# Kernel tuning notes

Measured on AMD Instinct MI355X. Metric: run time of the kernel, lower is better.

The kernel has to match this reference:

```python
import jax, jax.numpy as jnp
import numpy as np


def _skew_relative(QE):
    # QE: [B, H, N, 2N-1] -> [B, H, N, N] relative-position skew (Music-Transformer style)
    B, H, N, L = QE.shape  # L == 2N - 1
    x = jnp.pad(QE, ((0, 0), (0, 0), (0, 0), (0, 1))).reshape(B, H, N * (L + 1))
    x = jnp.pad(x, ((0, 0), (0, 0), (0, N - 1))).reshape(B, H, N + 1, 2 * N - 1)
    return x[:, :, :N, -N:]


def setup_inputs() -> dict:
    key = jax.random.key(0)
    ks = jax.random.split(key, 8)
    B, N, D, H, dh = 8, 1024, 512, 8, 64
    W_SCALE = 0.02
    return {
        "x": jax.random.normal(ks[0], (B, N, D), jnp.float32),
        "phase": jax.random.uniform(ks[1], (B, H, N, 1), jnp.float32),
        "E_rel": jax.random.normal(ks[2], (2 * N - 1, dh), jnp.float32) * 0.05,
        "W_q": jax.random.normal(ks[3], (H * dh, D), jnp.float32) * W_SCALE,
        "W_k": jax.random.normal(ks[4], (H * dh, D), jnp.float32) * W_SCALE,
        "W_v": jax.random.normal(ks[5], (H * dh, D), jnp.float32) * W_SCALE,
        "W_o": jax.random.normal(ks[6], (D, H * dh), jnp.float32) * W_SCALE,
        "b_o": jnp.zeros((D,), jnp.float32),
    }


def reference(x, phase, E_rel, W_q, W_k, W_v, W_o, b_o):
    B, N, _ = x.shape
    H = phase.shape[1]
    dh = W_q.shape[0] // H
    scale = 1.0 / (dh ** 0.5)

    def heads(W):  # [B,N,H*dh] -> [B,H,N,dh]
        return (x @ W.T).reshape(B, N, H, dh).transpose(0, 2, 1, 3)

    Q, K, V = heads(W_q), heads(W_k), heads(W_v)
    attn = jnp.einsum('bhnd,bhmd->bhnm', Q, K)
    attn = attn + _skew_relative(jnp.einsum('bhnd,ld->bhnl', Q, E_rel))
    attn = jax.nn.softmax(attn * scale, axis=-1)
    out = jnp.einsum('bhnm,bhmd->bhnd', attn, V) * phase  # phase-modulated AV
    out = out.transpose(0, 2, 1, 3).reshape(B, N, H * dh)
    return out @ W_o.T + b_o  # dropout is identity in eval mode
```

## Files before the change

### kernel.cpp

```cpp
#include <hip/hip_runtime.h>


typedef __bf16 bf16x8 __attribute__((ext_vector_type(8)));
typedef __bf16 bf16x4 __attribute__((ext_vector_type(4)));
typedef float  f32x4  __attribute__((ext_vector_type(4)));
typedef float  f32x16 __attribute__((ext_vector_type(16)));

#if __has_builtin(__builtin_amdgcn_exp2f)
#define EXP2(x) __builtin_amdgcn_exp2f(x)
#else
#define EXP2(x) exp2f(x)
#endif

#define QSCALE 0.18033688011f

#define GLOAD_LDS16(g, l)                                                      \
    __builtin_amdgcn_global_load_lds(                                          \
        (const __attribute__((address_space(1))) unsigned int*)(g),            \
        (__attribute__((address_space(3))) unsigned int*)(l), 16, 0, 0)


__global__ __launch_bounds__(256) void cvt_all(const float* __restrict__ x,
                                               const float* __restrict__ E,
                                               const float* __restrict__ wq,
                                               const float* __restrict__ wk,
                                               const float* __restrict__ wv,
                                               const float* __restrict__ wo,
                                               __bf16* __restrict__ xb,
                                               __bf16* __restrict__ Ef,
                                               __bf16* __restrict__ wqkv,
                                               __bf16* __restrict__ wob) {
    int i = blockIdx.x * 256 + threadIdx.x;
    if (i >= 1081328 ? i < 1343472 : i < 1048576) {
        const float* s; __bf16* d; int off;
        if      (i < 1048576) { s = x;  d = xb;            off = i; }
        else if (i < 1146864) { s = wq; d = wqkv;          off = i - 1081328; }
        else if (i < 1212400) { s = wk; d = wqkv + 262144; off = i - 1146864; }
        else if (i < 1277936) { s = wv; d = wqkv + 524288; off = i - 1212400; }
        else                  { s = wo; d = wob;           off = i - 1277936; }
        float4 v = *(const float4*)(s + (size_t)off * 4);
        bf16x4 o;
        o[0] = (__bf16)v.x; o[1] = (__bf16)v.y; o[2] = (__bf16)v.z; o[3] = (__bf16)v.w;
        *(bf16x4*)(d + (size_t)off * 4) = o;
    } else if (i >= 1048576 && i < 1081328) {
        int off = i - 1048576;
        float4 v = *(const float4*)(E + (size_t)off * 4);
        int e0i = off * 4;
        int l = e0i >> 6, d0 = e0i & 63;
        int t32 = l >> 5, cq = l & 31, ks = d0 >> 4, hf = (d0 >> 3) & 1, j = d0 & 7;
        bf16x4 o;
        o[0] = (__bf16)v.x; o[1] = (__bf16)v.y; o[2] = (__bf16)v.z; o[3] = (__bf16)v.w;
        *(bf16x4*)(Ef + ((size_t)((t32 * 4 + ks) * 64) + hf * 32 + cq) * 8 + j) = o;
    }
}

__global__ __launch_bounds__(256) void gemm_qkv(const __bf16* __restrict__ X,
                                                const __bf16* __restrict__ W,
                                                __bf16* __restrict__ Qb,
                                                __bf16* __restrict__ Kf,
                                                __bf16* __restrict__ Vf) {
    __shared__ __bf16 Xs[128][64];
    __shared__ __bf16 Ws[128][64];
    const int tid = threadIdx.x;
    const int wave = tid >> 6, lane = tid & 63;
    const int col = lane & 15, quad = lane >> 4;
    const int m_base = blockIdx.x * 128;
    const int j_base = blockIdx.y * 128;
    const bool qk = (j_base < 1024);
    const int wm = (wave & 1) * 64;
    const int wn = (wave >> 1) * 64;
    const f32x4 fz = {0.f, 0.f, 0.f, 0.f};
    f32x4 acc[4][4];
#pragma unroll
    for (int i = 0; i < 4; ++i)
#pragma unroll
        for (int j = 0; j < 4; ++j) acc[i][j] = fz;

    for (int k0 = 0; k0 < 512; k0 += 64) {
#pragma unroll
        for (int p = 0; p < 4; ++p) {
            int s = tid + p * 256;
            int row = s >> 3, cc = (s & 7) * 8;
            GLOAD_LDS16(X + (size_t)(m_base + row) * 512 + k0 + cc, &Xs[0][0] + (size_t)s * 8);
            GLOAD_LDS16(W + (size_t)(j_base + row) * 512 + k0 + cc, &Ws[0][0] + (size_t)s * 8);
        }
        __syncthreads();
#pragma unroll
        for (int kk = 0; kk < 64; kk += 32) {
            bf16x8 xa[4], wb[4];
#pragma unroll
            for (int i = 0; i < 4; ++i) xa[i] = *(const bf16x8*)(&Xs[wm + i * 16 + col][kk + quad * 8]);
#pragma unroll
            for (int j = 0; j < 4; ++j) wb[j] = *(const bf16x8*)(&Ws[wn + j * 16 + col][kk + quad * 8]);
            if (qk) {
#pragma unroll
                for (int i = 0; i < 4; ++i)
#pragma unroll
                    for (int j = 0; j < 4; ++j)
                        acc[i][j] = __builtin_amdgcn_mfma_f32_16x16x32_bf16(wb[i], xa[j], acc[i][j], 0, 0, 0);
            } else {
#pragma unroll
                for (int i = 0; i < 4; ++i)
#pragma unroll
                    for (int j = 0; j < 4; ++j)
                        acc[i][j] = __builtin_amdgcn_mfma_f32_16x16x32_bf16(xa[i], wb[j], acc[i][j], 0, 0, 0);
            }
        }
        __syncthreads();
    }
    if (qk) {
#pragma unroll
        for (int i = 0; i < 4; ++i) {
#pragma unroll
            for (int j = 0; j < 4; ++j) {
                int jabs = j_base + wn + i * 16 + quad * 4;
                int m = m_base + wm + j * 16 + col;
                int b_ = m >> 10, n = m & 1023;
                int rem = jabs & 511, h = rem >> 6, d = rem & 63;
                bf16x4 v;
                if (jabs < 512) {
                    v[0] = (__bf16)(acc[i][j][0] * QSCALE);
                    v[1] = (__bf16)(acc[i][j][1] * QSCALE);
                    v[2] = (__bf16)(acc[i][j][2] * QSCALE);
                    v[3] = (__bf16)(acc[i][j][3] * QSCALE);
                    *(bf16x4*)(Qb + (((size_t)b_ * 8 + h) * 1024 + n) * 64 + d) = v;
                } else {
                    v[0] = (__bf16)acc[i][j][0]; v[1] = (__bf16)acc[i][j][1];
                    v[2] = (__bf16)acc[i][j][2]; v[3] = (__bf16)acc[i][j][3];
                    int t32 = n >> 5, cq = n & 31, ks = d >> 4, hf = (d >> 3) & 1, jj = d & 7;
                    *(bf16x4*)(Kf + (size_t)(b_ * 8 + h) * 65536 +
                               ((size_t)((t32 * 4 + ks) * 64) + hf * 32 + cq) * 8 + jj) = v;
                }
            }
        }
    } else {
#pragma unroll
        for (int i = 0; i < 4; ++i) {
#pragma unroll
            for (int j = 0; j < 4; ++j) {
                int m = m_base + wm + i * 16 + quad * 4;
                int b_ = m >> 10, n = m & 1023;
                int jabs = j_base + wn + j * 16 + col;
                int rem = jabs & 511, h = rem >> 6, d = rem & 63;
                int t64 = n >> 6, ks = (n >> 4) & 3, hf = (n >> 3) & 1, jj = n & 7;
                int dhalf = d >> 5, cq = d & 31;
                bf16x4 v;
                v[0] = (__bf16)acc[i][j][0]; v[1] = (__bf16)acc[i][j][1];
                v[2] = (__bf16)acc[i][j][2]; v[3] = (__bf16)acc[i][j][3];
                *(bf16x4*)(Vf + (size_t)(b_ * 8 + h) * 65536 +
                           ((size_t)(((t64 * 4 + ks) * 2 + dhalf) * 64) + hf * 32 + cq) * 8 + jj) = v;
            }
        }
    }
}

__global__ __launch_bounds__(128) void flash_kernel(const __bf16* __restrict__ Qb,
                                                    const __bf16* __restrict__ Kf,
                                                    const __bf16* __restrict__ Vf,
                                                    const __bf16* __restrict__ Ef,
                                                    const float* __restrict__ phase,
                                                    __bf16* __restrict__ Ob) {
    const int bh = blockIdx.y;
    const int n0 = blockIdx.x * 64;
    const int w = threadIdx.x >> 6, lane = threadIdx.x & 63;
    const int colq = lane & 31, half = lane >> 5;
    const int nbase = n0 + w * 32;

    __shared__ __bf16 Pw[2][32][72];

    f32x16 z16;
#pragma unroll
    for (int i = 0; i < 16; ++i) z16[i] = 0.f;

    bf16x8 a_q[4];
#pragma unroll
    for (int ks = 0; ks < 4; ++ks)
        a_q[ks] = *(const bf16x8*)(Qb + ((size_t)bh * 1024 + nbase + colq) * 64 + ks * 16 + half * 8);

    f32x16 o0 = z16, o1 = z16;
    float rowsum[16];
#pragma unroll
    for (int i = 0; i < 16; ++i) rowsum[i] = 0.f;

    const __bf16* Kfb = Kf + (size_t)bh * 65536;
    const __bf16* Vfb = Vf + (size_t)bh * 65536;

    const int te0 = (992 - nbase) >> 5;

    float shA[16];
    {
        f32x16 qeA = z16;
#pragma unroll
        for (int ks = 0; ks < 4; ++ks) {
            bf16x8 e = *(const bf16x8*)(Ef + ((size_t)((te0 * 4 + ks) * 64) + lane) * 8);
            qeA = __builtin_amdgcn_mfma_f32_32x32x16_bf16(a_q[ks], e, qeA, 0, 0, 0);
        }
#pragma unroll
        for (int r = 0; r < 16; ++r) {
            int row = (r & 3) + 8 * (r >> 2) + 4 * half;
            int tt = colq + 31 - row;
            int src = (tt & 31) | (half << 5);
            shA[r] = __shfl(qeA[r], src, 64);
        }
    }

#pragma unroll 1
    for (int t = 0; t < 16; ++t) {
        const int m0 = t * 64;
        const int t32 = m0 >> 5;
        const int teB = te0 + 2 * t + 1;
        f32x16 qeB = z16, qeC = z16, s0 = z16, s1 = z16;
#pragma unroll
        for (int ks = 0; ks < 4; ++ks) {
            bf16x8 e1 = *(const bf16x8*)(Ef + ((size_t)((teB * 4 + ks) * 64) + lane) * 8);
            bf16x8 e2 = *(const bf16x8*)(Ef + ((size_t)(((teB + 1) * 4 + ks) * 64) + lane) * 8);
            bf16x8 k0 = *(const bf16x8*)(Kfb + ((size_t)((t32 * 4 + ks) * 64) + lane) * 8);
            bf16x8 k1 = *(const bf16x8*)(Kfb + ((size_t)(((t32 + 1) * 4 + ks) * 64) + lane) * 8);
            qeB = __builtin_amdgcn_mfma_f32_32x32x16_bf16(a_q[ks], e1, qeB, 0, 0, 0);
            qeC = __builtin_amdgcn_mfma_f32_32x32x16_bf16(a_q[ks], e2, qeC, 0, 0, 0);
            s0  = __builtin_amdgcn_mfma_f32_32x32x16_bf16(a_q[ks], k0, s0, 0, 0, 0);
            s1  = __builtin_amdgcn_mfma_f32_32x32x16_bf16(a_q[ks], k1, s1, 0, 0, 0);
        }
#pragma unroll
        for (int r = 0; r < 16; ++r) {
            int row = (r & 3) + 8 * (r >> 2) + 4 * half;
            int tt = colq + 31 - row;
            int src = (tt & 31) | (half << 5);
            float shB = __shfl(qeB[r], src, 64);
            float shC = __shfl(qeC[r], src, 64);
            bool sel = (tt >= 32);
            float rel0 = sel ? shB : shA[r];
            float rel1 = sel ? shC : shB;
            float p0 = EXP2(s0[r] + rel0);
            float p1 = EXP2(s1[r] + rel1);
            rowsum[r] += p0 + p1;
            Pw[w][row][colq]      = (__bf16)p0;
            Pw[w][row][32 + colq] = (__bf16)p1;
            shA[r] = shC;
        }
        asm volatile("s_waitcnt lgkmcnt(0)" ::: "memory");
#pragma unroll
        for (int ks = 0; ks < 4; ++ks) {
            bf16x8 pa = *(const bf16x8*)(&Pw[w][colq][ks * 16 + half * 8]);
            bf16x8 v0 = *(const bf16x8*)(Vfb + ((size_t)(((t * 4 + ks) * 2 + 0) * 64) + lane) * 8);
            bf16x8 v1 = *(const bf16x8*)(Vfb + ((size_t)(((t * 4 + ks) * 2 + 1) * 64) + lane) * 8);
            o0 = __builtin_amdgcn_mfma_f32_32x32x16_bf16(pa, v0, o0, 0, 0, 0);
            o1 = __builtin_amdgcn_mfma_f32_32x32x16_bf16(pa, v1, o1, 0, 0, 0);
        }
        asm volatile("" ::: "memory");
    }

    const int b_ = bh >> 3, hh = bh & 7;
#pragma unroll
    for (int r = 0; r < 16; ++r) {
        float l = rowsum[r];
        l += __shfl_xor(l, 1, 32);
        l += __shfl_xor(l, 2, 32);
        l += __shfl_xor(l, 4, 32);
        l += __shfl_xor(l, 8, 32);
        l += __shfl_xor(l, 16, 32);
        int row = (r & 3) + 8 * (r >> 2) + 4 * half;
        float f = phase[(size_t)bh * 1024 + nbase + row] / l;
        Pw[w][row][colq]      = (__bf16)(o0[r] * f);
        Pw[w][row][32 + colq] = (__bf16)(o1[r] * f);
    }
    asm volatile("s_waitcnt lgkmcnt(0)" ::: "memory");
    {
        int row = lane >> 1, dseg = lane & 1;
        bf16x8 u0 = *(const bf16x8*)(&Pw[w][row][dseg * 32]);
        bf16x8 u1 = *(const bf16x8*)(&Pw[w][row][dseg * 32 + 8]);
        bf16x8 u2 = *(const bf16x8*)(&Pw[w][row][dseg * 32 + 16]);
        bf16x8 u3 = *(const bf16x8*)(&Pw[w][row][dseg * 32 + 24]);
        size_t obase = ((size_t)b_ * 1024 + nbase + row) * 512 + hh * 64 + dseg * 32;
        *(bf16x8*)(Ob + obase)      = u0;
        *(bf16x8*)(Ob + obase + 8)  = u1;
        *(bf16x8*)(Ob + obase + 16) = u2;
        *(bf16x8*)(Ob + obase + 24) = u3;
    }
}

__global__ __launch_bounds__(256) void gemm_out(const __bf16* __restrict__ X,
                                                const __bf16* __restrict__ W,
                                                const float* __restrict__ bo,
                                                float* __restrict__ out) {
    __shared__ __bf16 Xs[128][64];
    __shared__ __bf16 Ws[64][64];
    const int tid = threadIdx.x;
    const int wave = tid >> 6, lane = tid & 63;
    const int col = lane & 15, quad = lane >> 4;
    const int m_base = blockIdx.x * 128;
    const int j_base = blockIdx.y * 64;
    const int wm = (wave & 1) * 64;
    const int wn = (wave >> 1) * 32;
    const f32x4 fz = {0.f, 0.f, 0.f, 0.f};
    f32x4 acc[2][4];
#pragma unroll
    for (int i = 0; i < 2; ++i)
#pragma unroll
        for (int j = 0; j < 4; ++j) acc[i][j] = fz;

    for (int k0 = 0; k0 < 512; k0 += 64) {
#pragma unroll
        for (int p = 0; p < 4; ++p) {
            int s = tid + p * 256;
            int row = s >> 3, cc = (s & 7) * 8;
            GLOAD_LDS16(X + (size_t)(m_base + row) * 512 + k0 + cc, &Xs[0][0] + (size_t)s * 8);
        }
#pragma unroll
        for (int p = 0; p < 2; ++p) {
            int s = tid + p * 256;
            int row = s >> 3, cc = (s & 7) * 8;
            GLOAD_LDS16(W + (size_t)(j_base + row) * 512 + k0 + cc, &Ws[0][0] + (size_t)s * 8);
        }
        __syncthreads();
#pragma unroll
        for (int kk = 0; kk < 64; kk += 32) {
            bf16x8 xa[4], wb[2];
#pragma unroll
            for (int j = 0; j < 4; ++j) xa[j] = *(const bf16x8*)(&Xs[wm + j * 16 + col][kk + quad * 8]);
#pragma unroll
            for (int i = 0; i < 2; ++i) wb[i] = *(const bf16x8*)(&Ws[wn + i * 16 + col][kk + quad * 8]);
#pragma unroll
            for (int i = 0; i < 2; ++i)
#pragma unroll
                for (int j = 0; j < 4; ++j)
                    acc[i][j] = __builtin_amdgcn_mfma_f32_16x16x32_bf16(wb[i], xa[j], acc[i][j], 0, 0, 0);
        }
        __syncthreads();
    }
#pragma unroll
    for (int i = 0; i < 2; ++i) {
#pragma unroll
        for (int j = 0; j < 4; ++j) {
            int jabs = j_base + wn + i * 16 + quad * 4;
            int m = m_base + wm + j * 16 + col;
            f32x4 bv = *(const f32x4*)(bo + jabs);
            f32x4 o = acc[i][j] + bv;
            *(f32x4*)(out + (size_t)m * 512 + jabs) = o;
        }
    }
}

extern "C" void kernel_launch(void* const* d_in, const int* in_sizes, int n_in,
                              void* d_out, int out_size, void* d_ws, size_t ws_size,
                              hipStream_t stream) {
    (void)in_sizes; (void)n_in; (void)out_size; (void)ws_size;
    const float* x     = (const float*)d_in[0];
    const float* phase = (const float*)d_in[1];
    const float* E_rel = (const float*)d_in[2];
    const float* W_q   = (const float*)d_in[3];
    const float* W_k   = (const float*)d_in[4];
    const float* W_v   = (const float*)d_in[5];
    const float* W_o   = (const float*)d_in[6];
    const float* b_o   = (const float*)d_in[7];
    float* out = (float*)d_out;

    char* ws = (char*)d_ws;
    __bf16* xb   = (__bf16*)(ws);
    __bf16* wqkv = (__bf16*)(ws + 8388608);
    __bf16* wob  = (__bf16*)(ws + 9961472);
    __bf16* Ef   = (__bf16*)(ws + 10485760);
    __bf16* Qb   = (__bf16*)(ws + 10747904);
    __bf16* Kf   = (__bf16*)(ws + 19136512);
    __bf16* Vf   = (__bf16*)(ws + 27525120);
    __bf16* Ob   = (__bf16*)(ws + 35913728);

    cvt_all<<<dim3(5249), dim3(256), 0, stream>>>(x, E_rel, W_q, W_k, W_v, W_o,
                                                  xb, Ef, wqkv, wob);
    gemm_qkv<<<dim3(64, 12), dim3(256), 0, stream>>>(xb, wqkv, Qb, Kf, Vf);
    flash_kernel<<<dim3(16, 64), dim3(128), 0, stream>>>(Qb, Kf, Vf, Ef, phase, Ob);
    gemm_out<<<dim3(64, 8), dim3(256), 0, stream>>>(Ob, wob, b_o, out);
}
```

Baseline: 183.1 us.

## Software-pipeline K loads one tile ahead in flash kernel with register double buffering

Restructures the flash attention loop into a manually unrolled pair of half-steps. K fragments for the next tile are prefetched into alternating register buffers while the current QK MFMAs run, and E/V loads are issued early so their latency overlaps compute. It also adds a launch-bounds minimum of 2 blocks per CU. The cost is higher register pressure, which could cause spills or lower occupancy.

Measured after the change: 170.8 us. 6.7% less time.

```diff
diff --git a/kernel.cpp b/kernel.cpp
--- a/kernel.cpp
+++ b/kernel.cpp
@@ -154,12 +154,71 @@
     }
 }
 
-__global__ __launch_bounds__(128) void flash_kernel(const __bf16* __restrict__ Qb,
-                                                    const __bf16* __restrict__ Kf,
-                                                    const __bf16* __restrict__ Vf,
-                                                    const __bf16* __restrict__ Ef,
-                                                    const float* __restrict__ phase,
-                                                    __bf16* __restrict__ Ob) {
+#define FLASH_HALF(T, KC0, KC1, KN0, KN1)                                              \
+  {                                                                                    \
+    const int t_ = (T);                                                                \
+    const int teB_ = te0 + 2 * t_ + 1;                                                 \
+    bf16x8 e1f[4], e2f[4], v0f[4], v1f[4];                                             \
+    _Pragma("unroll")                                                                  \
+    for (int ks = 0; ks < 4; ++ks) {                                                   \
+      e1f[ks] = *(const bf16x8*)(Ef + ((size_t)((teB_ * 4 + ks) * 64) + lane) * 8);    \
+      e2f[ks] = *(const bf16x8*)(Ef + ((size_t)(((teB_ + 1) * 4 + ks) * 64) + lane) * 8); \
+    }                                                                                  \
+    _Pragma("unroll")                                                                  \
+    for (int ks = 0; ks < 4; ++ks) {                                                   \
+      v0f[ks] = *(const bf16x8*)(Vfb + ((size_t)(((t_ * 4 + ks) * 2 + 0) * 64) + lane) * 8); \
+      v1f[ks] = *(const bf16x8*)(Vfb + ((size_t)(((t_ * 4 + ks) * 2 + 1) * 64) + lane) * 8); \
+    }                                                                                  \
+    f32x16 qeB = z16, qeC = z16, s0 = z16, s1 = z16;                                   \
+    _Pragma("unroll")                                                                  \
+    for (int ks = 0; ks < 4; ++ks) {                                                   \
+      s0 = __builtin_amdgcn_mfma_f32_32x32x16_bf16(a_q[ks], KC0[ks], s0, 0, 0, 0);     \
+      s1 = __builtin_amdgcn_mfma_f32_32x32x16_bf16(a_q[ks], KC1[ks], s1, 0, 0, 0);     \
+    }                                                                                  \
+    const int t32n_ = (((T) + 1) & 15) * 2;                                            \
+    _Pragma("unroll")                                                                  \
+    for (int ks = 0; ks < 4; ++ks) {                                                   \
+      KN0[ks] = *(const bf16x8*)(Kfb + ((size_t)((t32n_ * 4 + ks) * 64) + lane) * 8);  \
+      KN1[ks] = *(const bf16x8*)(Kfb + ((size_t)(((t32n_ + 1) * 4 + ks) * 64) + lane) * 8); \
+    }                                                                                  \
+    _Pragma("unroll")                                                                  \
+    for (int ks = 0; ks < 4; ++ks) {                                                   \
+      qeB = __builtin_amdgcn_mfma_f32_32x32x16_bf16(a_q[ks], e1f[ks], qeB, 0, 0, 0);   \
+      qeC = __builtin_amdgcn_mfma_f32_32x32x16_bf16(a_q[ks], e2f[ks], qeC, 0, 0, 0);   \
+    }                                                                                  \
+    _Pragma("unroll")                                                                  \
+    for (int r = 0; r < 16; ++r) {                                                     \
+      int row = (r & 3) + 8 * (r >> 2) + 4 * half;                                     \
+      int tt = colq + 31 - row;                                                        \
+      int src = (tt & 31) | (half << 5);                                               \
+      float shB = __shfl(qeB[r], src, 64);                                             \
+      float shC = __shfl(qeC[r], src, 64);                                             \
+      bool sel = (tt >= 32);                                                           \
+      float rel0 = sel ? shB : shA[r];                                                 \
+      float rel1 = sel ? shC : shB;                                                    \
+      float p0 = EXP2(s0[r] + rel0);                                                   \
+      float p1 = EXP2(s1[r] + rel1);                                                   \
+      rowsum[r] += p0 + p1;                                                            \
+      Pw[w][row][colq]      = (__bf16)p0;                                              \
+      Pw[w][row][32 + colq] = (__bf16)p1;                                              \
+      shA[r] = shC;                                                                    \
+    }                                                                                  \
+    asm volatile("s_waitcnt lgkmcnt(0)" ::: "memory");                                 \
+    _Pragma("unroll")                                                                  \
+    for (int ks = 0; ks < 4; ++ks) {                                                   \
+      bf16x8 pa = *(const bf16x8*)(&Pw[w][colq][ks * 16 + half * 8]);                  \
+      o0 = __builtin_amdgcn_mfma_f32_32x32x16_bf16(pa, v0f[ks], o0, 0, 0, 0);          \
+      o1 = __builtin_amdgcn_mfma_f32_32x32x16_bf16(pa, v1f[ks], o1, 0, 0, 0);          \
+    }                                                                                  \
+    asm volatile("" ::: "memory");                                                     \
+  }
+
+__global__ __launch_bounds__(128, 2) void flash_kernel(const __bf16* __restrict__ Qb,
+                                                       const __bf16* __restrict__ Kf,
+                                                       const __bf16* __restrict__ Vf,
+                                                       const __bf16* __restrict__ Ef,
+                                                       const float* __restrict__ phase,
+                                                       __bf16* __restrict__ Ob) {
     const int bh = blockIdx.y;
     const int n0 = blockIdx.x * 64;
     const int w = threadIdx.x >> 6, lane = threadIdx.x & 63;
@@ -187,6 +246,13 @@
 
     const int te0 = (992 - nbase) >> 5;
 
+    bf16x8 kA0[4], kA1[4], kB0[4], kB1[4];
+#pragma unroll
+    for (int ks = 0; ks < 4; ++ks) {
+        kA0[ks] = *(const bf16x8*)(Kfb + ((size_t)((0 * 4 + ks) * 64) + lane) * 8);
+        kA1[ks] = *(const bf16x8*)(Kfb + ((size_t)((1 * 4 + ks) * 64) + lane) * 8);
+    }
+
     float shA[16];
     {
         f32x16 qeA = z16;
@@ -205,49 +271,9 @@
     }
 
 #pragma unroll 1
-    for (int t = 0; t < 16; ++t) {
-        const int m0 = t * 64;
-        const int t32 = m0 >> 5;
-        const int teB = te0 + 2 * t + 1;
-        f32x16 qeB = z16, qeC = z16, s0 = z16, s1 = z16;
-#pragma unroll
-        for (int ks = 0; ks < 4; ++ks) {
-            bf16x8 e1 = *(const bf16x8*)(Ef + ((size_t)((teB * 4 + ks) * 64) + lane) * 8);
-            bf16x8 e2 = *(const bf16x8*)(Ef + ((size_t)(((teB + 1) * 4 + ks) * 64) + lane) * 8);
-            bf16x8 k0 = *(const bf16x8*)(Kfb + ((size_t)((t32 * 4 + ks) * 64) + lane) * 8);
-            bf16x8 k1 = *(const bf16x8*)(Kfb + ((size_t)(((t32 + 1) * 4 + ks) * 64) + lane) * 8);
-            qeB = __builtin_amdgcn_mfma_f32_32x32x16_bf16(a_q[ks], e1, qeB, 0, 0, 0);
-            qeC = __builtin_amdgcn_mfma_f32_32x32x16_bf16(a_q[ks], e2, qeC, 0, 0, 0);
-            s0  = __builtin_amdgcn_mfma_f32_32x32x16_bf16(a_q[ks], k0, s0, 0, 0, 0);
-            s1  = __builtin_amdgcn_mfma_f32_32x32x16_bf16(a_q[ks], k1, s1, 0, 0, 0);
-        }
-#pragma unroll
-        for (int r = 0; r < 16; ++r) {
-            int row = (r & 3) + 8 * (r >> 2) + 4 * half;
-            int tt = colq + 31 - row;
-            int src = (tt & 31) | (half << 5);
-            float shB = __shfl(qeB[r], src, 64);
-            float shC = __shfl(qeC[r], src, 64);
-            bool sel = (tt >= 32);
-            float rel0 = sel ? shB : shA[r];
-            float rel1 = sel ? shC : shB;
-            float p0 = EXP2(s0[r] + rel0);
-            float p1 = EXP2(s1[r] + rel1);
-            rowsum[r] += p0 + p1;
-            Pw[w][row][colq]      = (__bf16)p0;
-            Pw[w][row][32 + colq] = (__bf16)p1;
-            shA[r] = shC;
-        }
-        asm volatile("s_waitcnt lgkmcnt(0)" ::: "memory");
-#pragma unroll
-        for (int ks = 0; ks < 4; ++ks) {
-            bf16x8 pa = *(const bf16x8*)(&Pw[w][colq][ks * 16 + half * 8]);
-            bf16x8 v0 = *(const bf16x8*)(Vfb + ((size_t)(((t * 4 + ks) * 2 + 0) * 64) + lane) * 8);
-            bf16x8 v1 = *(const bf16x8*)(Vfb + ((size_t)(((t * 4 + ks) * 2 + 1) * 64) + lane) * 8);
-            o0 = __builtin_amdgcn_mfma_f32_32x32x16_bf16(pa, v0, o0, 0, 0, 0);
-            o1 = __builtin_amdgcn_mfma_f32_32x32x16_bf16(pa, v1, o1, 0, 0, 0);
-        }
-        asm volatile("" ::: "memory");
+    for (int tt2 = 0; tt2 < 8; ++tt2) {
+        FLASH_HALF(2 * tt2,     kA0, kA1, kB0, kB1)
+        FLASH_HALF(2 * tt2 + 1, kB0, kB1, kA0, kA1)
     }
 
     const int b_ = bh >> 3, hh = bh & 7;
```
